# Kernel optimization log

Hardware: AMD Instinct MI355X
Metric: run time of the kernel (lower is better)

Reference implementation:

```python
import jax, jax.numpy as jnp
import numpy as np

B, T, D = 8, 2048, 256
K, CS = 4, 1024  # num_codebooks, codebook_size


def setup_inputs() -> dict:
    key = jax.random.key(0)
    k_z, k_cb = jax.random.split(key)
    z = jax.random.normal(k_z, (B, T, D), dtype=jnp.float32)
    # original initializes each codebook with jax.random.uniform
    codebooks = jax.random.uniform(k_cb, (K, CS, D), dtype=jnp.float32)
    return {"z": z, "codebooks": codebooks}


def _rvq(z, codebooks):
    def step(residual, cb):
        # GEMM-based squared L2 distance: ||r||^2 - 2 r.c + ||c||^2.
        # ||r||^2 is constant over the codebook axis -> drop it for argmin.
        dist = jnp.sum(cb * cb, axis=-1)[None, None, :] \
            - 2.0 * jnp.einsum('btd,cd->btc', residual, cb)  # [B,T,CS]
        idx = jnp.argmin(dist, axis=-1)          # [B,T]
        q = cb[idx]                              # [B,T,D] gather
        z_q = residual + jax.lax.stop_gradient(q - residual)  # STE per stage
        return residual - z_q, (z_q, idx)

    _, (quants, indices) = jax.lax.scan(step, z, codebooks)
    z_q_final = jnp.sum(quants, axis=0)          # sum over stages
    z_q_final = z + jax.lax.stop_gradient(z_q_final - z)  # outer STE
    all_indices = jnp.moveaxis(indices, 0, -1)   # [B,T,K]
    return z_q_final, all_indices


def reference(z, codebooks):
    return _rvq(z, codebooks)
```

## Files before the change

kernel.cpp:

```cpp
#include <hip/hip_runtime.h>
#include <hip/hip_bf16.h>

#define DD 256
#define KK 4
#define CSZ 1024
#define NROWS 16384
#define TM 64
#define NTHR 1024
#define TAU 0.5f
#define MAXC 192

typedef __attribute__((ext_vector_type(8))) short bf16x8;
typedef __attribute__((ext_vector_type(4))) float f32x4;

__device__ __forceinline__ short f2bf(float f) {
    __hip_bfloat16 h = __float2bfloat16(f);
    return (short)__builtin_bit_cast(unsigned short, h);
}
__device__ __forceinline__ unsigned long long enc_d(double d) {
    unsigned long long u = __double_as_longlong(d);
    return (u & 0x8000000000000000ull) ? ~u : (u | 0x8000000000000000ull);
}

__global__ __launch_bounds__(256) void cb_pack(const float* __restrict__ cb,
                                               short* __restrict__ packed) {
    int idx  = blockIdx.x * 256 + threadIdx.x;
    int lane = idx & 63;
    int kk   = (idx >> 6) & 7;
    int tg   = idx >> 9;
    int k    = tg >> 6;
    int ctg  = tg & 63;
    int c    = ctg * 16 + (lane & 15);
    int d0   = kk * 32 + (lane >> 4) * 8;
    const float* src = cb + ((size_t)(k * CSZ + c)) * DD + d0;
    short* dst = packed + (size_t)idx * 8;
#pragma unroll
    for (int j = 0; j < 8; ++j) dst[j] = f2bf(src[j]);
}

__global__ __launch_bounds__(256) void cnorm_kernel(const float* __restrict__ cb,
                                                    double* __restrict__ cn_d,
                                                    float* __restrict__ cn_f) {
    int wv = threadIdx.x >> 6, l = threadIdx.x & 63;
    int e = blockIdx.x * 4 + wv;
    float4 v = *(const float4*)(cb + (size_t)e * DD + l * 4);
    double s = (double)v.x * (double)v.x + (double)v.y * (double)v.y
             + (double)v.z * (double)v.z + (double)v.w * (double)v.w;
#pragma unroll
    for (int off = 32; off > 0; off >>= 1) s += __shfl_xor(s, off, 64);
    if (l == 0) { cn_d[e] = s; cn_f[e] = (float)s; }
}

#define LOADB(Bv, CNv, t_) {                                          \
    const short* bp_ = pkk + (size_t)(t_) * 4096 + l * 8;             \
    _Pragma("unroll")                                                 \
    for (int kk = 0; kk < 8; ++kk)                                    \
        Bv[kk] = *(const bf16x8*)(bp_ + kk * 512);                    \
    CNv = cnfk[(t_) * 16 + l15]; }

#define KUPD(dval) {                                                  \
    float dc_ = fmaxf((dval), 0.f);                                   \
    unsigned kx_ = (__builtin_bit_cast(unsigned, dc_) & 0xFFFFFC00u)  \
                   | (unsigned)cE_;                                   \
    unsigned mx_ = (b0[reg] > kx_) ? b0[reg] : kx_;                   \
    b0[reg] = (b0[reg] < kx_) ? b0[reg] : kx_;                        \
    b1[reg] = (b1[reg] < mx_) ? b1[reg] : mx_; }

#define TILE1(Bv, CNv, t_) {                                          \
    f32x4 ac = {0.f,0.f,0.f,0.f};                                     \
    _Pragma("unroll")                                                 \
    for (int kk = 0; kk < 8; ++kk)                                    \
        ac = __builtin_amdgcn_mfma_f32_16x16x32_bf16(A[kk], Bv[kk], ac, 0,0,0); \
    const int cE_ = (t_) * 16 + l15;                                  \
    _Pragma("unroll")                                                 \
    for (int reg = 0; reg < 4; ++reg) {                               \
        KUPD(fmaf(-2.f, ac[reg], CNv));                               \
    } }

__global__ __launch_bounds__(NTHR, 1) void rvq_kernel(const float* __restrict__ z,
                                                  const float* __restrict__ cb,
                                                  const short* __restrict__ packed,
                                                  const double* __restrict__ cn_d,
                                                  const float* __restrict__ cn_f,
                                                  int* __restrict__ idx_ws,
                                                  float* __restrict__ out) {
    __shared__ double res_d[TM][DD + 1];
    __shared__ unsigned wrowmin[16][TM];
    __shared__ int cand[MAXC];
    __shared__ unsigned long long rowkey[2][TM];
    __shared__ int ncand;

    const int tid = threadIdx.x;
    const int l   = tid & 63;
    const int wv  = tid >> 6;
    const int rt  = wv & 3;
    const int sg  = wv >> 2;
    const int l15 = l & 15;
    const int q   = l >> 4;
    const int q8  = q * 8;
    const int row0 = blockIdx.x * TM;
    const int qrow = tid >> 8;
    const int hd   = tid & 255;

#pragma unroll 4
    for (int it = 0; it < TM / 4; ++it) {
        int r = it * 4 + qrow;
        res_d[r][hd] = (double)z[(size_t)(row0 + r) * DD + hd];
    }
    if (tid < TM) { rowkey[0][tid] = ~0ull; rowkey[1][tid] = ~0ull; }
    if (tid == 0) ncand = 0;
    __syncthreads();

    for (int k = 0; k < KK; ++k) {
        const int kb = k & 1;
        bf16x8 A[8];
#pragma unroll
        for (int kk = 0; kk < 8; ++kk) {
            const double* rp = &res_d[rt * 16 + l15][kk * 32 + q8];
#pragma unroll
            for (int j = 0; j < 8; ++j)
                A[kk][j] = f2bf((float)rp[j]);
        }

        const short* __restrict__ pkk  = packed + (size_t)k * CSZ * DD;
        const float* __restrict__ cnfk = cn_f + k * CSZ;
        unsigned b0[4], b1[4];
#pragma unroll
        for (int reg = 0; reg < 4; ++reg) { b0[reg] = ~0u; b1[reg] = ~0u; }

        {
            bf16x8 Bx[8];
            float cnX;
#pragma unroll 1
            for (int t = sg * 16; t < sg * 16 + 16; ++t) {
                LOADB(Bx, cnX, t);
                TILE1(Bx, cnX, t);
            }
        }

#pragma unroll
        for (int reg = 0; reg < 4; ++reg) {
            unsigned m = b0[reg];
            m = min(m, (unsigned)__shfl_xor((int)m, 1, 64));
            m = min(m, (unsigned)__shfl_xor((int)m, 2, 64));
            m = min(m, (unsigned)__shfl_xor((int)m, 4, 64));
            m = min(m, (unsigned)__shfl_xor((int)m, 8, 64));
            if (l15 == 0) wrowmin[wv][rt * 16 + q * 4 + reg] = m;
        }
        __syncthreads();

#pragma unroll
        for (int reg = 0; reg < 4; ++reg) {
            const int row = rt * 16 + q * 4 + reg;
            unsigned rk = min(min(wrowmin[rt][row], wrowmin[rt + 4][row]),
                              min(wrowmin[rt + 8][row], wrowmin[rt + 12][row]));
            float thrf = __builtin_bit_cast(float, rk | 0x3FFu) + TAU;
            unsigned tkey = (__builtin_bit_cast(unsigned, thrf) & 0xFFFFFC00u) | 0x3FFu;
            if (b0[reg] <= tkey) {
                int sl = atomicAdd(&ncand, 1);
                if (sl < MAXC) cand[sl] = row | ((int)(b0[reg] & 0x3FFu) << 16);
            }
            if (b1[reg] <= tkey) {
                int sl = atomicAdd(&ncand, 1);
                if (sl < MAXC) cand[sl] = row | ((int)(b1[reg] & 0x3FFu) << 16);
            }
        }
        __syncthreads();

        const int nc = (ncand < MAXC) ? ncand : MAXC;
        const float* __restrict__ cbk   = cb + (size_t)k * CSZ * DD;
        const double* __restrict__ cndk = cn_d + k * CSZ;
        const int g = tid >> 4;
        for (int i = g; i < nc; i += 64) {
            int rc  = cand[i];
            int row = rc & 0xFFFF;
            int c   = rc >> 16;
            const float* crow = cbk + (size_t)c * DD;
            double p = 0.0;
#pragma unroll
            for (int ii = 0; ii < 16; ++ii)
                p += res_d[row][ii * 16 + l15] * (double)crow[ii * 16 + l15];
            p += __shfl_xor(p, 1, 64);
            p += __shfl_xor(p, 2, 64);
            p += __shfl_xor(p, 4, 64);
            p += __shfl_xor(p, 8, 64);
            if (l15 == 0) {
                double dist = cndk[c] - 2.0 * p;
                unsigned long long key =
                    (enc_d(dist) & 0xFFFFFFFFFFFFFC00ull) | (unsigned long long)c;
                atomicMin(&rowkey[kb][row], key);
            }
        }
        __syncthreads();

        if (tid < TM)
            idx_ws[(size_t)(row0 + tid) * KK + k] = (int)(rowkey[kb][tid] & 1023ull);
#pragma unroll 4
        for (int it = 0; it < TM / 4; ++it) {
            int r = it * 4 + qrow;
            int c = (int)(rowkey[kb][r] & 1023ull);
            double qv = (double)cbk[(size_t)c * DD + hd];
            double rd = res_d[r][hd];
            double s  = qv - rd;
            double zq = rd + s;
            res_d[r][hd] = rd - zq;
        }
        if (tid < TM) rowkey[kb ^ 1][tid] = ~0ull;
        if (tid == 0) ncand = 0;
        __syncthreads();
    }

#pragma unroll 4
    for (int it = 0; it < TM / 4; ++it) {
        int r = it * 4 + qrow;
        size_t o = (size_t)(row0 + r) * DD + hd;
        out[o] = (float)((double)z[o] - res_d[r][hd]);
    }
}

__global__ __launch_bounds__(256) void idx_write(const int* __restrict__ idx_ws,
                                                 float* __restrict__ out) {
    int i = blockIdx.x * 256 + threadIdx.x;
    out[(long)NROWS * DD + i] = (float)idx_ws[i];
}

extern "C" void kernel_launch(void* const* d_in, const int* in_sizes, int n_in,
                              void* d_out, int out_size, void* d_ws, size_t ws_size,
                              hipStream_t stream) {
    (void)in_sizes; (void)n_in; (void)out_size; (void)ws_size;
    const float* z  = (const float*)d_in[0];
    const float* cb = (const float*)d_in[1];

    char* ws = (char*)d_ws;
    short*  packed = (short*)ws;
    double* cn_d  = (double*)(ws + (size_t)2 * 1024 * 1024);
    float*  cn_f  = (float*)(ws + (size_t)2 * 1024 * 1024 + 32 * 1024);
    int*    idxs  = (int*)(ws + (size_t)2 * 1024 * 1024 + 48 * 1024);
    float* out = (float*)d_out;

    cb_pack<<<(KK * 64 * 8 * 64) / 256, 256, 0, stream>>>(cb, packed);
    cnorm_kernel<<<(KK * CSZ) / 4, 256, 0, stream>>>(cb, cn_d, cn_f);
    rvq_kernel<<<NROWS / TM, NTHR, 0, stream>>>(z, cb, packed, cn_d, cn_f, idxs, out);
    idx_write<<<(NROWS * KK) / 256, 256, 0, stream>>>(idxs, out);
}
```

Baseline: 119.2 us.

## Shrink row tile to 16 with split float+bf16 residual in transposed LDS

Reduces the block from 64 rows and 1024 threads to 16 rows and 256 threads, so each wave scans a quarter of the codebook for the same 16 rows and many more blocks run concurrently. The double-precision residual in shared memory is replaced by a transposed float high part plus a bf16 low part, which cuts LDS footprint so more blocks fit per CU. The index write is fused into the main kernel, removing a separate launch. In exchange, the same codebook tiles are reloaded by four times as many blocks, and the residual carries slightly less precision than full double, which could change argmin ties in the exact refinement step.

```diff
diff --git a/kernel.cpp b/kernel.cpp
--- a/kernel.cpp
+++ b/kernel.cpp
@@ -5,10 +5,10 @@
 #define KK 4
 #define CSZ 1024
 #define NROWS 16384
-#define TM 64
-#define NTHR 1024
+#define TM 16
+#define NTHR 256
 #define TAU 0.5f
-#define MAXC 192
+#define MAXC 128
 
 typedef __attribute__((ext_vector_type(8))) short bf16x8;
 typedef __attribute__((ext_vector_type(4))) float f32x4;
@@ -16,6 +16,10 @@
 __device__ __forceinline__ short f2bf(float f) {
     __hip_bfloat16 h = __float2bfloat16(f);
     return (short)__builtin_bit_cast(unsigned short, h);
+}
+__device__ __forceinline__ float bf2f(short s) {
+    unsigned u = ((unsigned)(unsigned short)s) << 16;
+    return __builtin_bit_cast(float, u);
 }
 __device__ __forceinline__ unsigned long long enc_d(double d) {
     unsigned long long u = __double_as_longlong(d);
@@ -77,15 +81,15 @@
         KUPD(fmaf(-2.f, ac[reg], CNv));                               \
     } }
 
-__global__ __launch_bounds__(NTHR, 1) void rvq_kernel(const float* __restrict__ z,
+__global__ __launch_bounds__(NTHR) void rvq_kernel(const float* __restrict__ z,
                                                   const float* __restrict__ cb,
                                                   const short* __restrict__ packed,
                                                   const double* __restrict__ cn_d,
                                                   const float* __restrict__ cn_f,
-                                                  int* __restrict__ idx_ws,
                                                   float* __restrict__ out) {
-    __shared__ double res_d[TM][DD + 1];
-    __shared__ unsigned wrowmin[16][TM];
+    __shared__ float res_hi[DD][TM + 1];
+    __shared__ short res_lo[DD][TM + 2];
+    __shared__ unsigned wrowmin[4][TM];
     __shared__ int cand[MAXC];
     __shared__ unsigned long long rowkey[2][TM];
     __shared__ int ncand;
@@ -93,19 +97,15 @@
     const int tid = threadIdx.x;
     const int l   = tid & 63;
     const int wv  = tid >> 6;
-    const int rt  = wv & 3;
-    const int sg  = wv >> 2;
     const int l15 = l & 15;
     const int q   = l >> 4;
     const int q8  = q * 8;
     const int row0 = blockIdx.x * TM;
-    const int qrow = tid >> 8;
-    const int hd   = tid & 255;
 
 #pragma unroll 4
-    for (int it = 0; it < TM / 4; ++it) {
-        int r = it * 4 + qrow;
-        res_d[r][hd] = (double)z[(size_t)(row0 + r) * DD + hd];
+    for (int r = 0; r < TM; ++r) {
+        res_hi[tid][r] = z[(size_t)(row0 + r) * DD + tid];
+        res_lo[tid][r] = 0;
     }
     if (tid < TM) { rowkey[0][tid] = ~0ull; rowkey[1][tid] = ~0ull; }
     if (tid == 0) ncand = 0;
@@ -116,10 +116,11 @@
         bf16x8 A[8];
 #pragma unroll
         for (int kk = 0; kk < 8; ++kk) {
-            const double* rp = &res_d[rt * 16 + l15][kk * 32 + q8];
+            bf16x8 a;
 #pragma unroll
             for (int j = 0; j < 8; ++j)
-                A[kk][j] = f2bf((float)rp[j]);
+                a[j] = f2bf(res_hi[kk * 32 + q8 + j][l15]);
+            A[kk] = a;
         }
 
         const short* __restrict__ pkk  = packed + (size_t)k * CSZ * DD;
@@ -132,7 +133,7 @@
             bf16x8 Bx[8];
             float cnX;
 #pragma unroll 1
-            for (int t = sg * 16; t < sg * 16 + 16; ++t) {
+            for (int t = wv * 16; t < wv * 16 + 16; ++t) {
                 LOADB(Bx, cnX, t);
                 TILE1(Bx, cnX, t);
             }
@@ -145,15 +146,15 @@
             m = min(m, (unsigned)__shfl_xor((int)m, 2, 64));
             m = min(m, (unsigned)__shfl_xor((int)m, 4, 64));
             m = min(m, (unsigned)__shfl_xor((int)m, 8, 64));
-            if (l15 == 0) wrowmin[wv][rt * 16 + q * 4 + reg] = m;
+            if (l15 == 0) wrowmin[wv][q * 4 + reg] = m;
         }
         __syncthreads();
 
 #pragma unroll
         for (int reg = 0; reg < 4; ++reg) {
-            const int row = rt * 16 + q * 4 + reg;
-            unsigned rk = min(min(wrowmin[rt][row], wrowmin[rt + 4][row]),
-                              min(wrowmin[rt + 8][row], wrowmin[rt + 12][row]));
+            const int row = q * 4 + reg;
+            unsigned rk = min(min(wrowmin[0][row], wrowmin[1][row]),
+                              min(wrowmin[2][row], wrowmin[3][row]));
             float thrf = __builtin_bit_cast(float, rk | 0x3FFu) + TAU;
             unsigned tkey = (__builtin_bit_cast(unsigned, thrf) & 0xFFFFFC00u) | 0x3FFu;
             if (b0[reg] <= tkey) {
@@ -171,15 +172,18 @@
         const float* __restrict__ cbk   = cb + (size_t)k * CSZ * DD;
         const double* __restrict__ cndk = cn_d + k * CSZ;
         const int g = tid >> 4;
-        for (int i = g; i < nc; i += 64) {
+        for (int i = g; i < nc; i += 16) {
             int rc  = cand[i];
             int row = rc & 0xFFFF;
             int c   = rc >> 16;
             const float* crow = cbk + (size_t)c * DD;
             double p = 0.0;
 #pragma unroll
-            for (int ii = 0; ii < 16; ++ii)
-                p += res_d[row][ii * 16 + l15] * (double)crow[ii * 16 + l15];
+            for (int ii = 0; ii < 16; ++ii) {
+                int d = ii * 16 + l15;
+                double rv = (double)res_hi[d][row] + (double)bf2f(res_lo[d][row]);
+                p += rv * (double)crow[d];
+            }
             p += __shfl_xor(p, 1, 64);
             p += __shfl_xor(p, 2, 64);
             p += __shfl_xor(p, 4, 64);
@@ -194,16 +198,19 @@
         __syncthreads();
 
         if (tid < TM)
-            idx_ws[(size_t)(row0 + tid) * KK + k] = (int)(rowkey[kb][tid] & 1023ull);
+            out[(size_t)NROWS * DD + (size_t)(row0 + tid) * KK + k] =
+                (float)(int)(rowkey[kb][tid] & 1023ull);
 #pragma unroll 4
-        for (int it = 0; it < TM / 4; ++it) {
-            int r = it * 4 + qrow;
+        for (int r = 0; r < TM; ++r) {
             int c = (int)(rowkey[kb][r] & 1023ull);
-            double qv = (double)cbk[(size_t)c * DD + hd];
-            double rd = res_d[r][hd];
+            double qv = (double)cbk[(size_t)c * DD + tid];
+            double rd = (double)res_hi[tid][r] + (double)bf2f(res_lo[tid][r]);
             double s  = qv - rd;
             double zq = rd + s;
-            res_d[r][hd] = rd - zq;
+            double rn = rd - zq;
+            float hi = (float)rn;
+            res_hi[tid][r] = hi;
+            res_lo[tid][r] = f2bf((float)(rn - (double)hi));
         }
         if (tid < TM) rowkey[kb ^ 1][tid] = ~0ull;
         if (tid == 0) ncand = 0;
@@ -211,17 +218,11 @@
     }
 
 #pragma unroll 4
-    for (int it = 0; it < TM / 4; ++it) {
-        int r = it * 4 + qrow;
-        size_t o = (size_t)(row0 + r) * DD + hd;
-        out[o] = (float)((double)z[o] - res_d[r][hd]);
+    for (int r = 0; r < TM; ++r) {
+        size_t o = (size_t)(row0 + r) * DD + tid;
+        double rv = (double)res_hi[tid][r] + (double)bf2f(res_lo[tid][r]);
+        out[o] = (float)((double)z[o] - rv);
     }
-}
-
-__global__ __launch_bounds__(256) void idx_write(const int* __restrict__ idx_ws,
-                                                 float* __restrict__ out) {
-    int i = blockIdx.x * 256 + threadIdx.x;
-    out[(long)NROWS * DD + i] = (float)idx_ws[i];
 }
 
 extern "C" void kernel_launch(void* const* d_in, const int* in_sizes, int n_in,
@@ -235,11 +236,9 @@
     short*  packed = (short*)ws;
     double* cn_d  = (double*)(ws + (size_t)2 * 1024 * 1024);
     float*  cn_f  = (float*)(ws + (size_t)2 * 1024 * 1024 + 32 * 1024);
-    int*    idxs  = (int*)(ws + (size_t)2 * 1024 * 1024 + 48 * 1024);
     float* out = (float*)d_out;
 
     cb_pack<<<(KK * 64 * 8 * 64) / 256, 256, 0, stream>>>(cb, packed);
     cnorm_kernel<<<(KK * CSZ) / 4, 256, 0, stream>>>(cb, cn_d, cn_f);
-    rvq_kernel<<<NROWS / TM, NTHR, 0, stream>>>(z, cb, packed, cn_d, cn_f, idxs, out);
-    idx_write<<<(NROWS * KK) / 256, 256, 0, stream>>>(idxs, out);
-}
+    rvq_kernel<<<NROWS / TM, NTHR, 0, stream>>>(z, cb, packed, cn_d, cn_f, out);
+}
```

Measured after the change: 106.4 us. 10.8% less time.
